# Optimization experiments

Hardware: AMD Instinct MI355X
Metric: run time of the kernel (lower is better)

The kernel has to match this reference:

```python
import jax, jax.numpy as jnp
import numpy as np

N = 20000   # nodes per frame
T = 16      # frames
E = 320000  # edges per frame
C = 128     # in_channels
H = 128     # hidden_channels
P = 100000  # decode pairs


def setup_inputs() -> dict:
    key = jax.random.key(0)
    ks = jax.random.split(key, 12)
    s = 1.0 / np.sqrt(H)
    return {
        "x_seq": jax.random.normal(ks[0], (T, N, C), jnp.float32),
        "edge_index": jax.random.randint(ks[1], (T, 2, E), 0, N, jnp.int32),
        "edge_pairs": jax.random.randint(ks[2], (2, P), 0, N, jnp.int32),
        "W1": jax.random.normal(ks[3], (C, H), jnp.float32) * s,
        "b1": jnp.zeros((H,), jnp.float32),
        "W2": jax.random.normal(ks[4], (H, H), jnp.float32) * s,
        "b2": jnp.zeros((H,), jnp.float32),
        "W3": jax.random.normal(ks[5], (H, H), jnp.float32) * s,
        "b3": jnp.zeros((H,), jnp.float32),
        "w_ih": jax.random.normal(ks[6], (3 * H, H), jnp.float32) * s,
        "w_hh": jax.random.normal(ks[7], (3 * H, H), jnp.float32) * s,
        "b_ih": jnp.zeros((3 * H,), jnp.float32),
        "b_hh": jnp.zeros((3 * H,), jnp.float32),
    }


def _gcn(x, src, dst, W, b):
    # PyG GCNConv: h = x @ W; add self-loops; D^{-1/2}(A+I)D^{-1/2} aggregation; + b
    h = x @ W                                   # [N, H]
    ones = jnp.ones(src.shape[0], x.dtype)
    deg = jax.ops.segment_sum(ones, dst, num_segments=N) + 1.0  # self-loop included
    dinv = jax.lax.rsqrt(deg)
    norm = dinv[src] * dinv[dst]                # [E]
    agg = jax.ops.segment_sum(h[src] * norm[:, None], dst, num_segments=N)
    agg = agg + h * (dinv * dinv)[:, None]      # self-loop message (norm = 1/deg)
    return agg + b


def reference(x_seq, edge_index, edge_pairs, W1, b1, W2, b2, W3, b3,
              w_ih, w_hh, b_ih, b_hh):
    def frame(_, inp):
        x, ei = inp
        src, dst = ei[0], ei[1]
        h = jax.nn.relu(_gcn(x, src, dst, W1, b1))
        h = jax.nn.relu(_gcn(h, src, dst, W2, b2))
        h = _gcn(h, src, dst, W3, b3)
        return None, h

    _, feats = jax.lax.scan(frame, None, (x_seq, edge_index))  # [T, N, H]

    # single-layer torch GRU over time; only final hidden state needed
    def gru_step(hprev, x_t):
        gi = x_t @ w_ih.T + b_ih                # [N, 3H]
        gh = hprev @ w_hh.T + b_hh
        i_r, i_z, i_n = jnp.split(gi, 3, axis=1)
        h_r, h_z, h_n = jnp.split(gh, 3, axis=1)
        r = jax.nn.sigmoid(i_r + h_r)
        z = jax.nn.sigmoid(i_z + h_z)
        n = jnp.tanh(i_n + r * h_n)
        h_new = (1.0 - z) * n + z * hprev
        return h_new, None

    h0 = jnp.zeros((N, H), x_seq.dtype)
    h_last, _ = jax.lax.scan(gru_step, h0, feats)  # [N, H]

    zs = h_last[edge_pairs[0]]                  # [P, H]
    zd = h_last[edge_pairs[1]]
    return jnp.sum(zs * zd, axis=1)             # [P]
```

## Files before the change

kernel.cpp:

```cpp
#include <hip/hip_runtime.h>
#include <hip/hip_bf16.h>

#define NN 20000
#define TT 16
#define EE 320000
#define CC 128
#define HH 128
#define PP 100000
#define QN (NN / 4)

typedef float  f32x4  __attribute__((ext_vector_type(4)));
typedef unsigned short ushort8v __attribute__((ext_vector_type(8)));
typedef unsigned u32x4 __attribute__((ext_vector_type(4)));
typedef _Float16 h2v __attribute__((ext_vector_type(2)));
typedef _Float16 h4v __attribute__((ext_vector_type(4)));
typedef _Float16 f16x8 __attribute__((ext_vector_type(8)));

union pk16 { unsigned u; _Float16 h[2]; };


__global__ void hist_all_k(const int* __restrict__ edge_index, int* __restrict__ cnt_all) {
    int b = blockIdx.x;
    int f = b & 15, chunk = b >> 4;
    const int* dst = edge_index + (size_t)f * 2 * EE + EE;
    int* cnt = cnt_all + f * NN;
    int base = chunk * 1024 + threadIdx.x;
#pragma unroll
    for (int i = 0; i < 4; ++i) {
        int e = base + i * 256;
        if (e < EE) {
            int d = __builtin_nontemporal_load(dst + e);
            atomicAdd(&cnt[d], 1);
        }
    }
}

__global__ __launch_bounds__(1024) void scan_all_k(const int* __restrict__ cnt_all,
                                                   int* __restrict__ offs_all,
                                                   float* __restrict__ dinv_all,
                                                   int* __restrict__ cursor_all) {
    __shared__ int part[1024];
    int f = blockIdx.x;
    const int* cnt = cnt_all + f * NN;
    int* offs = offs_all + f * (NN + 1);
    int t = threadIdx.x;
    int base = t * 20;
    int vals[20];
    int s = 0;
#pragma unroll
    for (int i = 0; i < 20; ++i) {
        int idx = base + i;
        int v = (idx < NN) ? cnt[idx] : 0;
        vals[i] = v; s += v;
    }
    part[t] = s;
    __syncthreads();
    for (int off = 1; off < 1024; off <<= 1) {
        int v = (t >= off) ? part[t - off] : 0;
        __syncthreads();
        part[t] += v;
        __syncthreads();
    }
    int run = part[t] - s;
#pragma unroll
    for (int i = 0; i < 20; ++i) {
        int idx = base + i;
        if (idx < NN) {
            offs[idx] = run;
            cursor_all[f * NN + idx] = f * EE + run;
            dinv_all[f * NN + idx] = rsqrtf((float)vals[i] + 1.0f);
            run += vals[i];
        }
    }
    if (t == 0) offs[NN] = EE;
}

__global__ void fill_all_k(const int* __restrict__ edge_index,
                           int* __restrict__ cursor_all,
                           unsigned short* __restrict__ csr_all) {
    int b = blockIdx.x;
    int f = b & 15, chunk = b >> 4;
    const int* src = edge_index + (size_t)f * 2 * EE;
    const int* dst = src + EE;
    int* cur = cursor_all + f * NN;
    int base = chunk * 1024 + threadIdx.x;
#pragma unroll
    for (int i = 0; i < 4; ++i) {
        int e = base + i * 256;
        if (e < EE) {
            int d = __builtin_nontemporal_load(dst + e);
            int s = __builtin_nontemporal_load(src + e);
            int pos = atomicAdd(&cur[d], 1);
            csr_all[pos] = (unsigned short)s;
        }
    }
}

__global__ void wprep_t_k(const float* __restrict__ W,
                          _Float16* __restrict__ oh,
                          _Float16* __restrict__ ol) {
    int i = blockIdx.x * blockDim.x + threadIdx.x;
    if (i >= 128 * 128) return;
    int n = i >> 7, k = i & 127;
    float v = W[k * 128 + n];
    _Float16 h = (_Float16)v;
    oh[i] = h;
    ol[i] = (_Float16)(v - (float)h);
}

__global__ void wprep_d_k(const float* __restrict__ w,
                          _Float16* __restrict__ oh,
                          _Float16* __restrict__ ol, int n) {
    int i = blockIdx.x * blockDim.x + threadIdx.x;
    if (i >= n) return;
    float v = w[i];
    _Float16 h = (_Float16)v;
    oh[i] = h;
    ol[i] = (_Float16)(v - (float)h);
}

__global__ __launch_bounds__(256) void scale_k(const float* __restrict__ x,
                                               const float* __restrict__ dinv_all,
                                               _Float16* __restrict__ g) {
    int idx = blockIdx.x * blockDim.x + threadIdx.x;
    int row = idx >> 5, q = idx & 31;
    const f32x4* xp = (const f32x4*)(x + (size_t)row * 128 + q * 4);
    f32x4 v = __builtin_nontemporal_load(xp);
    float d = dinv_all[row];
    h4v o;
    o.x = (_Float16)(v.x * d); o.y = (_Float16)(v.y * d);
    o.z = (_Float16)(v.z * d); o.w = (_Float16)(v.w * d);
    *(h4v*)(g + (size_t)row * 128 + q * 4) = o;
}

__global__ __launch_bounds__(128) void agg_half_k(const _Float16* __restrict__ g,
                                                  const unsigned short* __restrict__ csr_all,
                                                  const int* __restrict__ offs_all,
                                                  _Float16* __restrict__ a) {
    int b = blockIdx.x;
    int xcd = b & 7;
    int r1 = b >> 3;
    int grp = r1 % QN;
    int pass = r1 / QN;
    int f = xcd + ((pass & 1) << 3);
    int hoff = (pass >> 1) * 64;
    int t = threadIdx.x;
    int node = grp * 4 + (t >> 5);
    int lane = t & 31;
    const int* offs = offs_all + f * (NN + 1);
    const unsigned short* csr = csr_all + (size_t)f * EE;
    const _Float16* gf = g + (size_t)f * NN * HH + hoff + lane * 2;
    int beg = offs[node], end = offs[node + 1];
    float a0 = 0.f, a1 = 0.f;
    int e = beg;
    for (; e + 3 < end; e += 4) {
        int s0 = csr[e], s1 = csr[e + 1], s2 = csr[e + 2], s3 = csr[e + 3];
        h2v v0 = *(const h2v*)(gf + (size_t)s0 * HH);
        h2v v1 = *(const h2v*)(gf + (size_t)s1 * HH);
        h2v v2 = *(const h2v*)(gf + (size_t)s2 * HH);
        h2v v3 = *(const h2v*)(gf + (size_t)s3 * HH);
        a0 += ((float)v0.x + (float)v1.x) + ((float)v2.x + (float)v3.x);
        a1 += ((float)v0.y + (float)v1.y) + ((float)v2.y + (float)v3.y);
    }
    for (; e < end; ++e) {
        h2v v = *(const h2v*)(gf + (size_t)csr[e] * HH);
        a0 += (float)v.x; a1 += (float)v.y;
    }
    h2v vs = *(const h2v*)(gf + (size_t)node * HH);
    a0 += (float)vs.x; a1 += (float)vs.y;
    h2v r; r.x = (_Float16)a0; r.y = (_Float16)a1;
    *(h2v*)(a + ((size_t)f * NN + node) * HH + hoff + lane * 2) = r;
}

__global__ __launch_bounds__(256) void gemm_f16(const _Float16* __restrict__ A,
                                                const _Float16* __restrict__ Bh,
                                                const _Float16* __restrict__ Bl,
                                                _Float16* __restrict__ out,
                                                const float* __restrict__ rowscale,
                                                const float* __restrict__ bias,
                                                int M, int NC, int relu, int postscale) {
    __shared__ _Float16 As[64 * 72], Bhs[64 * 72], Bls[64 * 72];
    int t = threadIdx.x;
    int b = blockIdx.x;
    int xcd = b & 7, k = b >> 3;
    int row_t = xcd + ((k >> 1) << 3);
    int col_t = k & 1;
    int row0 = row_t * 64, col0 = col_t * 64;
    int w = t >> 6, lane = t & 63;
    int wm = (w & 1) * 32, wn = (w >> 1) * 32;
    int lm = lane & 15, lq = lane >> 4;
    f32x4 acc[2][2] = {};

    for (int ks = 0; ks < 2; ++ks) {
        if (ks) __syncthreads();
#pragma unroll
        for (int p = 0; p < 2; ++p) {
            int s = t + p * 256;
            int r = s >> 3, c8 = s & 7;
            int gr = row0 + r;
            ushort8v va = {};
            if (gr < M)
                va = *(const ushort8v*)(A + (size_t)gr * 128 + ks * 64 + c8 * 8);
            *(ushort8v*)&As[r * 72 + c8 * 8] = va;
            *(ushort8v*)&Bhs[r * 72 + c8 * 8] =
                *(const ushort8v*)(Bh + (size_t)(col0 + r) * 128 + ks * 64 + c8 * 8);
            *(ushort8v*)&Bls[r * 72 + c8 * 8] =
                *(const ushort8v*)(Bl + (size_t)(col0 + r) * 128 + ks * 64 + c8 * 8);
        }
        __syncthreads();
#pragma unroll
        for (int q = 0; q < 2; ++q) {
            int ko = q * 32 + lq * 8;
            f16x8 av[2], bh[2], bl[2];
#pragma unroll
            for (int i = 0; i < 2; ++i)
                av[i] = *(const f16x8*)&As[(wm + i * 16 + lm) * 72 + ko];
#pragma unroll
            for (int j = 0; j < 2; ++j) {
                bh[j] = *(const f16x8*)&Bhs[(wn + j * 16 + lm) * 72 + ko];
                bl[j] = *(const f16x8*)&Bls[(wn + j * 16 + lm) * 72 + ko];
            }
#pragma unroll
            for (int i = 0; i < 2; ++i)
#pragma unroll
                for (int j = 0; j < 2; ++j) {
                    acc[i][j] = __builtin_amdgcn_mfma_f32_16x16x32_f16(av[i], bh[j], acc[i][j], 0, 0, 0);
                    acc[i][j] = __builtin_amdgcn_mfma_f32_16x16x32_f16(av[i], bl[j], acc[i][j], 0, 0, 0);
                }
        }
    }
#pragma unroll
    for (int i = 0; i < 2; ++i)
#pragma unroll
        for (int reg = 0; reg < 4; ++reg) {
            int gr = row0 + wm + i * 16 + lq * 4 + reg;
            if (gr < M) {
                float sc = rowscale ? rowscale[gr] : 1.0f;
#pragma unroll
                for (int j = 0; j < 2; ++j) {
                    int col = col0 + wn + j * 16 + lm;
                    float v = acc[i][j][reg];
                    if (rowscale) v *= sc;
                    v += bias[col];
                    if (relu) v = fmaxf(v, 0.f);
                    if (postscale) v *= sc;
                    out[(size_t)gr * NC + col] = (_Float16)v;
                }
            }
        }
}

__global__ __launch_bounds__(512, 1) void gru_all_k(const _Float16* __restrict__ F,
                                                    const _Float16* __restrict__ wihh,
                                                    const _Float16* __restrict__ wihl,
                                                    const _Float16* __restrict__ whhh,
                                                    const _Float16* __restrict__ whhl,
                                                    const float* __restrict__ b_ih,
                                                    const float* __restrict__ b_hh,
                                                    float* __restrict__ hgru) {
    __shared__ unsigned hs2[64 * 132];
    int t = threadIdx.x;
    int row0 = blockIdx.x * 64;
    for (int s = t; s < 64 * 132; s += 512) hs2[s] = 0u;

    int w = t >> 6, lane = t & 63;
    int lm = lane & 15, lq = lane >> 4;
    int h_idx = w * 16 + lm;
    float bsr = b_ih[h_idx] + b_hh[h_idx];
    float bsz = b_ih[h_idx + 128] + b_hh[h_idx + 128];
    float bni = b_ih[h_idx + 256];
    float bnh = b_hh[h_idx + 256];
    size_t wbase = (size_t)h_idx * 128 + lq * 8;
    const _Float16* Fb = F + (size_t)(row0 + lm) * 128 + lq * 8;
    bool rowok[4];
#pragma unroll
    for (int i = 0; i < 4; ++i) rowok[i] = (row0 + i * 16 + lm) < NN;

    char* hsb = (char*)hs2;

    for (int tt = 0; tt < TT; ++tt) {
        __syncthreads();
        const _Float16* Ft = Fb + (size_t)tt * NN * 128;

        f32x4 accr[4], accz[4], accni[4], accnh[4];
#pragma unroll
        for (int i = 0; i < 4; ++i) {
            accr[i] = (f32x4){0.f, 0.f, 0.f, 0.f};
            accz[i] = (f32x4){0.f, 0.f, 0.f, 0.f};
            accni[i] = (f32x4){0.f, 0.f, 0.f, 0.f};
            accnh[i] = (f32x4){0.f, 0.f, 0.f, 0.f};
        }

#pragma unroll
        for (int q = 0; q < 4; ++q) {
            size_t o = wbase + q * 32;
            f16x8 wr_h = *(const f16x8*)(wihh + o);
            f16x8 wr_l = *(const f16x8*)(wihl + o);
            f16x8 wz_h = *(const f16x8*)(wihh + o + 16384);
            f16x8 wz_l = *(const f16x8*)(wihl + o + 16384);
            f16x8 wn_h = *(const f16x8*)(wihh + o + 32768);
            f16x8 wn_l = *(const f16x8*)(wihl + o + 32768);
            f16x8 af[4];
#pragma unroll
            for (int i = 0; i < 4; ++i)
                af[i] = rowok[i] ? *(const f16x8*)(Ft + (size_t)i * 2048 + q * 32)
                                 : (f16x8){};
#pragma unroll
            for (int i = 0; i < 4; ++i) {
                accr[i]  = __builtin_amdgcn_mfma_f32_16x16x32_f16(af[i], wr_h, accr[i], 0, 0, 0);
                accr[i]  = __builtin_amdgcn_mfma_f32_16x16x32_f16(af[i], wr_l, accr[i], 0, 0, 0);
                accz[i]  = __builtin_amdgcn_mfma_f32_16x16x32_f16(af[i], wz_h, accz[i], 0, 0, 0);
                accz[i]  = __builtin_amdgcn_mfma_f32_16x16x32_f16(af[i], wz_l, accz[i], 0, 0, 0);
                accni[i] = __builtin_amdgcn_mfma_f32_16x16x32_f16(af[i], wn_h, accni[i], 0, 0, 0);
                accni[i] = __builtin_amdgcn_mfma_f32_16x16x32_f16(af[i], wn_l, accni[i], 0, 0, 0);
            }
        }

#pragma unroll
        for (int q = 0; q < 4; ++q) {
            size_t o = wbase + q * 32;
            f16x8 wr_h = *(const f16x8*)(whhh + o);
            f16x8 wr_l = *(const f16x8*)(whhl + o);
            f16x8 wz_h = *(const f16x8*)(whhh + o + 16384);
            f16x8 wz_l = *(const f16x8*)(whhl + o + 16384);
            f16x8 wn_h = *(const f16x8*)(whhh + o + 32768);
            f16x8 wn_l = *(const f16x8*)(whhl + o + 32768);
#pragma unroll
            for (int i = 0; i < 4; ++i) {
                int row = i * 16 + lm;
                int c0 = (q * 32 + lq * 8) * 4;
                int c1 = c0 + 16;
                int sw = (row & 7) << 4;
                u32x4 v0 = *(const u32x4*)(hsb + row * 528 + (c0 ^ sw));
                u32x4 v1 = *(const u32x4*)(hsb + row * 528 + (c1 ^ sw));
                f16x8 ah, al;
#pragma unroll
                for (int e = 0; e < 4; ++e) {
                    pk16 c; c.u = v0[e]; ah[e] = c.h[0]; al[e] = c.h[1];
                    pk16 d; d.u = v1[e]; ah[e + 4] = d.h[0]; al[e + 4] = d.h[1];
                }
                accr[i]  = __builtin_amdgcn_mfma_f32_16x16x32_f16(ah, wr_h, accr[i], 0, 0, 0);
                accr[i]  = __builtin_amdgcn_mfma_f32_16x16x32_f16(ah, wr_l, accr[i], 0, 0, 0);
                accr[i]  = __builtin_amdgcn_mfma_f32_16x16x32_f16(al, wr_h, accr[i], 0, 0, 0);
                accz[i]  = __builtin_amdgcn_mfma_f32_16x16x32_f16(ah, wz_h, accz[i], 0, 0, 0);
                accz[i]  = __builtin_amdgcn_mfma_f32_16x16x32_f16(ah, wz_l, accz[i], 0, 0, 0);
                accz[i]  = __builtin_amdgcn_mfma_f32_16x16x32_f16(al, wz_h, accz[i], 0, 0, 0);
                accnh[i] = __builtin_amdgcn_mfma_f32_16x16x32_f16(ah, wn_h, accnh[i], 0, 0, 0);
                accnh[i] = __builtin_amdgcn_mfma_f32_16x16x32_f16(ah, wn_l, accnh[i], 0, 0, 0);
                accnh[i] = __builtin_amdgcn_mfma_f32_16x16x32_f16(al, wn_h, accnh[i], 0, 0, 0);
            }
        }

#pragma unroll
        for (int i = 0; i < 4; ++i)
#pragma unroll
            for (int reg = 0; reg < 4; ++reg) {
                int row_l = i * 16 + lq * 4 + reg;
                pk16 c;
                c.u = *(const unsigned*)(hsb + row_l * 528 + ((h_idx * 4) ^ ((row_l & 7) << 4)));
                float hp = (float)c.h[0] + (float)c.h[1];
                float r = 1.f / (1.f + __expf(-(accr[i][reg] + bsr)));
                float z = 1.f / (1.f + __expf(-(accz[i][reg] + bsz)));
                float nv = tanhf(accni[i][reg] + bni + r * (accnh[i][reg] + bnh));
                accr[i][reg] = (1.f - z) * nv + z * hp;
            }
        __syncthreads();
#pragma unroll
        for (int i = 0; i < 4; ++i)
#pragma unroll
            for (int reg = 0; reg < 4; ++reg) {
                int row_l = i * 16 + lq * 4 + reg;
                float hv = accr[i][reg];
                _Float16 hi = (_Float16)hv;
                pk16 c; c.h[0] = hi; c.h[1] = (_Float16)(hv - (float)hi);
                *(unsigned*)(hsb + row_l * 528 + ((h_idx * 4) ^ ((row_l & 7) << 4))) = c.u;
                if (tt == TT - 1 && row0 + row_l < NN)
                    hgru[(size_t)(row0 + row_l) * 128 + h_idx] = hv;
            }
    }
}

__global__ __launch_bounds__(256) void decode_k(const float* __restrict__ hgru,
                                                const int* __restrict__ pairs,
                                                float* __restrict__ out) {
    int gid = blockIdx.x * blockDim.x + threadIdx.x;
    int w = gid >> 6;
    int lane = threadIdx.x & 63;
    if (w >= PP) return;
    int s = pairs[w], d = pairs[PP + w];
    const float* zs = hgru + (size_t)s * HH;
    const float* zd = hgru + (size_t)d * HH;
    float acc = zs[lane] * zd[lane] + zs[lane + 64] * zd[lane + 64];
#pragma unroll
    for (int off = 32; off > 0; off >>= 1) acc += __shfl_down(acc, off);
    if (lane == 0) out[w] = acc;
}

static inline size_t align256(size_t x) { return (x + 255) & ~(size_t)255; }

extern "C" void kernel_launch(void* const* d_in, const int* in_sizes, int n_in,
                              void* d_out, int out_size, void* d_ws, size_t ws_size,
                              hipStream_t stream) {
    const float* x_seq      = (const float*)d_in[0];
    const int*   edge_index = (const int*)d_in[1];
    const int*   edge_pairs = (const int*)d_in[2];
    const float* W1 = (const float*)d_in[3];
    const float* b1 = (const float*)d_in[4];
    const float* W2 = (const float*)d_in[5];
    const float* b2 = (const float*)d_in[6];
    const float* W3 = (const float*)d_in[7];
    const float* b3 = (const float*)d_in[8];
    const float* w_ih = (const float*)d_in[9];
    const float* w_hh = (const float*)d_in[10];
    const float* b_ih = (const float*)d_in[11];
    const float* b_hh = (const float*)d_in[12];

    const size_t MALL = (size_t)TT * NN;

    char* p = (char*)d_ws;
    int*   cnt_all    = (int*)p;   p += align256(MALL * sizeof(int));
    int*   offs_all   = (int*)p;   p += align256((size_t)TT * (NN + 1) * sizeof(int));
    int*   cursor_all = (int*)p;   p += align256(MALL * sizeof(int));
    float* dinv_all   = (float*)p; p += align256(MALL * sizeof(float));
    unsigned short* csr_all = (unsigned short*)p; p += align256((size_t)TT * EE * sizeof(unsigned short));
    _Float16* g   = (_Float16*)p;  p += align256(MALL * HH * sizeof(_Float16));
    _Float16* a   = (_Float16*)p;  p += align256(MALL * HH * sizeof(_Float16));
    _Float16* F   = (_Float16*)p;  p += align256(MALL * HH * sizeof(_Float16));
    float* hgru = (float*)p;       p += align256((size_t)NN * HH * sizeof(float));
    _Float16* W1h = (_Float16*)p; p += align256(128 * 128 * 2);
    _Float16* W1l = (_Float16*)p; p += align256(128 * 128 * 2);
    _Float16* W2h = (_Float16*)p; p += align256(128 * 128 * 2);
    _Float16* W2l = (_Float16*)p; p += align256(128 * 128 * 2);
    _Float16* W3h = (_Float16*)p; p += align256(128 * 128 * 2);
    _Float16* W3l = (_Float16*)p; p += align256(128 * 128 * 2);
    _Float16* wihh = (_Float16*)p; p += align256(384 * 128 * 2);
    _Float16* wihl = (_Float16*)p; p += align256(384 * 128 * 2);
    _Float16* whhh = (_Float16*)p; p += align256(384 * 128 * 2);
    _Float16* whhl = (_Float16*)p; p += align256(384 * 128 * 2);

    hipMemsetAsync(cnt_all, 0, MALL * sizeof(int), stream);

    wprep_t_k<<<64, 256, 0, stream>>>(W1, W1h, W1l);
    wprep_t_k<<<64, 256, 0, stream>>>(W2, W2h, W2l);
    wprep_t_k<<<64, 256, 0, stream>>>(W3, W3h, W3l);
    wprep_d_k<<<192, 256, 0, stream>>>(w_ih, wihh, wihl, 384 * 128);
    wprep_d_k<<<192, 256, 0, stream>>>(w_hh, whhh, whhl, 384 * 128);

    int ge = ((EE + 1023) / 1024) * TT;
    hist_all_k<<<ge, 256, 0, stream>>>(edge_index, cnt_all);
    scan_all_k<<<TT, 1024, 0, stream>>>(cnt_all, offs_all, dinv_all, cursor_all);
    fill_all_k<<<ge, 256, 0, stream>>>(edge_index, cursor_all, csr_all);

    scale_k<<<(int)(MALL * 32 / 256), 256, 0, stream>>>(x_seq, dinv_all, g);

    int gagg = 8 * QN * 4;
    int ggemm = 2 * (int)(MALL / 64);

    agg_half_k<<<gagg, 128, 0, stream>>>(g, csr_all, offs_all, a);
    gemm_f16<<<ggemm, 256, 0, stream>>>(a, W1h, W1l, g, dinv_all, b1, (int)MALL, 128, 1, 1);
    agg_half_k<<<gagg, 128, 0, stream>>>(g, csr_all, offs_all, a);
    gemm_f16<<<ggemm, 256, 0, stream>>>(a, W2h, W2l, g, dinv_all, b2, (int)MALL, 128, 1, 1);
    agg_half_k<<<gagg, 128, 0, stream>>>(g, csr_all, offs_all, a);
    gemm_f16<<<ggemm, 256, 0, stream>>>(a, W3h, W3l, F, dinv_all, b3, (int)MALL, 128, 0, 0);

    int gru_blocks = (NN + 63) / 64;
    gru_all_k<<<gru_blocks, 512, 0, stream>>>(F, wihh, wihl, whhh, whhl,
                                              b_ih, b_hh, hgru);

    decode_k<<<(PP * 64 + 255) / 256, 256, 0, stream>>>(hgru, edge_pairs, (float*)d_out);
}
```

Before: 1.925 ms.

## Stage GRU inputs in LDS in MFMA fragment order and pre-pack weights

GRU weights are pre-permuted on the device into a fragment-contiguous layout, so each lane's weight loads are fully coalesced 16-byte reads. Each timestep's feature tile is first loaded cooperatively with coalesced loads into shared memory, stored in MFMA fragment order, and then read per lane from there. The hidden-state buffer in shared memory uses the same fragment layout in place of the swizzled row layout. This trades an extra barrier and 16KB more LDS per step for fewer strided global loads.

```diff
diff --git a/kernel.cpp b/kernel.cpp
--- a/kernel.cpp
+++ b/kernel.cpp
@@ -108,15 +108,21 @@
     ol[i] = (_Float16)(v - (float)h);
 }
 
-__global__ void wprep_d_k(const float* __restrict__ w,
-                          _Float16* __restrict__ oh,
-                          _Float16* __restrict__ ol, int n) {
-    int i = blockIdx.x * blockDim.x + threadIdx.x;
-    if (i >= n) return;
-    float v = w[i];
-    _Float16 h = (_Float16)v;
-    oh[i] = h;
-    ol[i] = (_Float16)(v - (float)h);
+__global__ __launch_bounds__(256) void wprep_p_k(const float* __restrict__ wsrc,
+                                                 _Float16* __restrict__ oh,
+                                                 _Float16* __restrict__ ol) {
+    int u = blockIdx.x * blockDim.x + threadIdx.x;
+    if (u >= 6144) return;
+    int lane = u & 63, q = (u >> 6) & 3, wv = (u >> 8) & 7, g = u >> 11;
+    int lm = lane & 15, lq = lane >> 4;
+    const float* s = wsrc + (size_t)(g * 128 + wv * 16 + lm) * 128 + q * 32 + lq * 8;
+#pragma unroll
+    for (int e = 0; e < 8; ++e) {
+        float v = s[e];
+        _Float16 h = (_Float16)v;
+        oh[(size_t)u * 8 + e] = h;
+        ol[(size_t)u * 8 + e] = (_Float16)(v - (float)h);
+    }
 }
 
 __global__ __launch_bounds__(256) void scale_k(const float* __restrict__ x,
@@ -258,10 +264,11 @@
                                                     const float* __restrict__ b_ih,
                                                     const float* __restrict__ b_hh,
                                                     float* __restrict__ hgru) {
-    __shared__ unsigned hs2[64 * 132];
+    __shared__ unsigned hsu[8192];
+    __shared__ _Float16 fsu[8192];
     int t = threadIdx.x;
     int row0 = blockIdx.x * 64;
-    for (int s = t; s < 64 * 132; s += 512) hs2[s] = 0u;
+    for (int s = t; s < 8192; s += 512) hsu[s] = 0u;
 
     int w = t >> 6, lane = t & 63;
     int lm = lane & 15, lq = lane >> 4;
@@ -270,17 +277,23 @@
     float bsz = b_ih[h_idx + 128] + b_hh[h_idx + 128];
     float bni = b_ih[h_idx + 256];
     float bnh = b_hh[h_idx + 256];
-    size_t wbase = (size_t)h_idx * 128 + lq * 8;
-    const _Float16* Fb = F + (size_t)(row0 + lm) * 128 + lq * 8;
-    bool rowok[4];
-#pragma unroll
-    for (int i = 0; i < 4; ++i) rowok[i] = (row0 + i * 16 + lm) < NN;
-
-    char* hsb = (char*)hs2;
+    size_t wb = (size_t)w * 2048 + (size_t)lane * 8;
+    int qv = h_idx >> 5, lqv = (h_idx >> 3) & 3, ev = h_idx & 7;
 
     for (int tt = 0; tt < TT; ++tt) {
         __syncthreads();
-        const _Float16* Ft = Fb + (size_t)tt * NN * 128;
+        const _Float16* Ft = F + ((size_t)tt * NN + row0) * 128;
+#pragma unroll
+        for (int it = 0; it < 2; ++it) {
+            int s = t + it * 512;
+            int r = s >> 4, c8 = s & 15;
+            ushort8v val = {};
+            if (row0 + r < NN)
+                val = *(const ushort8v*)(Ft + (size_t)r * 128 + c8 * 8);
+            int fu = ((r >> 4) * 4 + (c8 >> 2)) * 64 + (c8 & 3) * 16 + (r & 15);
+            *(ushort8v*)(fsu + fu * 8) = val;
+        }
+        __syncthreads();
 
         f32x4 accr[4], accz[4], accni[4], accnh[4];
 #pragma unroll
@@ -293,32 +306,28 @@
 
 #pragma unroll
         for (int q = 0; q < 4; ++q) {
-            size_t o = wbase + q * 32;
+            size_t o = wb + q * 512;
             f16x8 wr_h = *(const f16x8*)(wihh + o);
             f16x8 wr_l = *(const f16x8*)(wihl + o);
             f16x8 wz_h = *(const f16x8*)(wihh + o + 16384);
             f16x8 wz_l = *(const f16x8*)(wihl + o + 16384);
             f16x8 wn_h = *(const f16x8*)(wihh + o + 32768);
             f16x8 wn_l = *(const f16x8*)(wihl + o + 32768);
-            f16x8 af[4];
-#pragma unroll
-            for (int i = 0; i < 4; ++i)
-                af[i] = rowok[i] ? *(const f16x8*)(Ft + (size_t)i * 2048 + q * 32)
-                                 : (f16x8){};
 #pragma unroll
             for (int i = 0; i < 4; ++i) {
-                accr[i]  = __builtin_amdgcn_mfma_f32_16x16x32_f16(af[i], wr_h, accr[i], 0, 0, 0);
-                accr[i]  = __builtin_amdgcn_mfma_f32_16x16x32_f16(af[i], wr_l, accr[i], 0, 0, 0);
-                accz[i]  = __builtin_amdgcn_mfma_f32_16x16x32_f16(af[i], wz_h, accz[i], 0, 0, 0);
-                accz[i]  = __builtin_amdgcn_mfma_f32_16x16x32_f16(af[i], wz_l, accz[i], 0, 0, 0);
-                accni[i] = __builtin_amdgcn_mfma_f32_16x16x32_f16(af[i], wn_h, accni[i], 0, 0, 0);
-                accni[i] = __builtin_amdgcn_mfma_f32_16x16x32_f16(af[i], wn_l, accni[i], 0, 0, 0);
+                f16x8 af = *(const f16x8*)(fsu + ((i * 4 + q) * 64 + lane) * 8);
+                accr[i]  = __builtin_amdgcn_mfma_f32_16x16x32_f16(af, wr_h, accr[i], 0, 0, 0);
+                accr[i]  = __builtin_amdgcn_mfma_f32_16x16x32_f16(af, wr_l, accr[i], 0, 0, 0);
+                accz[i]  = __builtin_amdgcn_mfma_f32_16x16x32_f16(af, wz_h, accz[i], 0, 0, 0);
+                accz[i]  = __builtin_amdgcn_mfma_f32_16x16x32_f16(af, wz_l, accz[i], 0, 0, 0);
+                accni[i] = __builtin_amdgcn_mfma_f32_16x16x32_f16(af, wn_h, accni[i], 0, 0, 0);
+                accni[i] = __builtin_amdgcn_mfma_f32_16x16x32_f16(af, wn_l, accni[i], 0, 0, 0);
             }
         }
 
 #pragma unroll
         for (int q = 0; q < 4; ++q) {
-            size_t o = wbase + q * 32;
+            size_t o = wb + q * 512;
             f16x8 wr_h = *(const f16x8*)(whhh + o);
             f16x8 wr_l = *(const f16x8*)(whhl + o);
             f16x8 wz_h = *(const f16x8*)(whhh + o + 16384);
@@ -327,12 +336,9 @@
             f16x8 wn_l = *(const f16x8*)(whhl + o + 32768);
 #pragma unroll
             for (int i = 0; i < 4; ++i) {
-                int row = i * 16 + lm;
-                int c0 = (q * 32 + lq * 8) * 4;
-                int c1 = c0 + 16;
-                int sw = (row & 7) << 4;
-                u32x4 v0 = *(const u32x4*)(hsb + row * 528 + (c0 ^ sw));
-                u32x4 v1 = *(const u32x4*)(hsb + row * 528 + (c1 ^ sw));
+                const unsigned* hp = hsu + ((i * 4 + q) * 64 + lane) * 8;
+                u32x4 v0 = *(const u32x4*)(hp);
+                u32x4 v1 = *(const u32x4*)(hp + 4);
                 f16x8 ah, al;
 #pragma unroll
                 for (int e = 0; e < 4; ++e) {
@@ -355,9 +361,8 @@
         for (int i = 0; i < 4; ++i)
 #pragma unroll
             for (int reg = 0; reg < 4; ++reg) {
-                int row_l = i * 16 + lq * 4 + reg;
-                pk16 c;
-                c.u = *(const unsigned*)(hsb + row_l * 528 + ((h_idx * 4) ^ ((row_l & 7) << 4)));
+                int u = (i * 4 + qv) * 64 + lqv * 16 + lq * 4 + reg;
+                pk16 c; c.u = hsu[u * 8 + ev];
                 float hp = (float)c.h[0] + (float)c.h[1];
                 float r = 1.f / (1.f + __expf(-(accr[i][reg] + bsr)));
                 float z = 1.f / (1.f + __expf(-(accz[i][reg] + bsz)));
@@ -369,13 +374,15 @@
         for (int i = 0; i < 4; ++i)
 #pragma unroll
             for (int reg = 0; reg < 4; ++reg) {
-                int row_l = i * 16 + lq * 4 + reg;
+                int u = (i * 4 + qv) * 64 + lqv * 16 + lq * 4 + reg;
                 float hv = accr[i][reg];
                 _Float16 hi = (_Float16)hv;
                 pk16 c; c.h[0] = hi; c.h[1] = (_Float16)(hv - (float)hi);
-                *(unsigned*)(hsb + row_l * 528 + ((h_idx * 4) ^ ((row_l & 7) << 4))) = c.u;
-                if (tt == TT - 1 && row0 + row_l < NN)
-                    hgru[(size_t)(row0 + row_l) * 128 + h_idx] = hv;
+                hsu[u * 8 + ev] = c.u;
+                if (tt == TT - 1) {
+                    int gr = row0 + i * 16 + lq * 4 + reg;
+                    if (gr < NN) hgru[(size_t)gr * 128 + h_idx] = hv;
+                }
             }
     }
 }
@@ -443,8 +450,8 @@
     wprep_t_k<<<64, 256, 0, stream>>>(W1, W1h, W1l);
     wprep_t_k<<<64, 256, 0, stream>>>(W2, W2h, W2l);
     wprep_t_k<<<64, 256, 0, stream>>>(W3, W3h, W3l);
-    wprep_d_k<<<192, 256, 0, stream>>>(w_ih, wihh, wihl, 384 * 128);
-    wprep_d_k<<<192, 256, 0, stream>>>(w_hh, whhh, whhl, 384 * 128);
+    wprep_p_k<<<24, 256, 0, stream>>>(w_ih, wihh, wihl);
+    wprep_p_k<<<24, 256, 0, stream>>>(w_hh, whhh, whhl);
 
     int ge = ((EE + 1023) / 1024) * TT;
     hist_all_k<<<ge, 256, 0, stream>>>(edge_index, cnt_all);
```

Result: faster. 1.728 ms (-10.2%).
